# Optimization experiments

Measured on AMD Instinct MI355X. Metric: run time of the kernel, lower is better.

Reference implementation:

```python
import jax, jax.numpy as jnp
import numpy as np

# Block structure (mirrors init_kwargs)
K = 8            # number of blocks
BLK = 1024       # per-block in/out width
TOTAL = K * BLK  # total_dim = 8192
INPUT_IDX = [(i * BLK, (i + 1) * BLK) for i in range(K)]
OUTPUT_IDX = [(((i + 1) % K) * BLK, ((i + 1) % K + 1) * BLK) for i in range(K)]
BATCH = 4096


def setup_inputs() -> dict:
    key = jax.random.key(0)
    k1, k2, k3, k4 = jax.random.split(key, 4)
    x = jax.random.normal(k1, (BATCH, TOTAL), dtype=jnp.float32)
    v = jax.random.normal(k2, (BATCH, TOTAL), dtype=jnp.float32)
    # Per-block Linear params; nn.Linear default init ~ U(-1/sqrt(in), 1/sqrt(in))
    bound = 1.0 / np.sqrt(BLK)
    W = jax.random.uniform(k3, (K, BLK, BLK), dtype=jnp.float32, minval=-bound, maxval=bound)  # [K, out, in]
    b = jax.random.uniform(k4, (K, BLK), dtype=jnp.float32, minval=-bound, maxval=bound)
    return {"x": x, "v": v, "W": W, "b": b}


def reference(x, v, W, b):
    # hidden = act(v)
    hidden = jnp.tanh(v)
    # All input blocks are a uniform partition -> batch the K small GEMMs as one grouped contraction.
    h = hidden.reshape(BATCH, K, BLK)                      # [B, K, in]
    y = jnp.einsum("bki,koi->bko", h, W) + b               # [B, K, out]
    # Scatter-accumulate each block output into its padded position, plus residual x.
    result = x
    for i, (o0, o1) in enumerate(OUTPUT_IDX):
        result = result.at[:, o0:o1].add(y[:, i])
    return result
```

## Files before the change

kernel.cpp:

```cpp
#include <hip/hip_runtime.h>
#include <hip/hip_bf16.h>
#include <stdint.h>

#define BATCH 4096
#define KGRP  8
#define BLK   1024
#define TOTAL 8192

typedef __attribute__((ext_vector_type(8))) short short8;
typedef __attribute__((ext_vector_type(4))) float f32x4;

#define AS1 __attribute__((address_space(1)))
#define AS3 __attribute__((address_space(3)))


__device__ __forceinline__ unsigned short f2bf(float f) {
    union { float f; uint32_t u; } c; c.f = f;
    uint32_t u = c.u;
    u += 0x7fffu + ((u >> 16) & 1u);
    return (unsigned short)(u >> 16);
}

__device__ __forceinline__ float fast_tanh(float x) {
    float e = __expf(2.0f * x);
    return 1.0f - 2.0f / (e + 1.0f);
}


__global__ void k_prep(const float4* __restrict__ v, ushort4* __restrict__ H,
                       const float4* __restrict__ W, ushort4* __restrict__ Wb) {
    const int b = blockIdx.x;
    if (b < 2048) {
        const int n4 = BATCH * TOTAL / 4;
        for (int i = b * 256 + threadIdx.x; i < n4; i += 2048 * 256) {
            float4 f = v[i];
            ushort4 o;
            o.x = f2bf(fast_tanh(f.x)); o.y = f2bf(fast_tanh(f.y));
            o.z = f2bf(fast_tanh(f.z)); o.w = f2bf(fast_tanh(f.w));
            H[i] = o;
        }
    } else {
        const int n4 = KGRP * BLK * BLK / 4;
        for (int i = (b - 2048) * 256 + threadIdx.x; i < n4; i += 512 * 256) {
            float4 f = W[i];
            ushort4 o;
            o.x = f2bf(f.x); o.y = f2bf(f.y); o.z = f2bf(f.z); o.w = f2bf(f.w);
            Wb[i] = o;
        }
    }
}


__device__ __forceinline__ void gload16(const unsigned short* src, char* dst) {
    __builtin_amdgcn_global_load_lds((const AS1 uint32_t*)src, (AS3 uint32_t*)dst, 16, 0, 0);
}

template<int N> __device__ __forceinline__ void waitvm() {
    if constexpr (N == 0)      asm volatile("s_waitcnt vmcnt(0)" ::: "memory");
    else if constexpr (N == 3) asm volatile("s_waitcnt vmcnt(3)" ::: "memory");
}

template<bool ST, int W, int CUR>
__device__ __forceinline__ void tile3(int kt, char* ldsp,
                                      uint32_t aRowB, uint32_t bRowB,
                                      f32x4 (*acc)[4],
                                      const unsigned short* Asrc, const unsigned short* Bsrc,
                                      uint32_t sdst) {
    constexpr uint32_t bufb = (uint32_t)(CUR * 24576);
    constexpr uint32_t stgb = (uint32_t)(((CUR + 2) % 3) * 24576);
    const char* Lb = ldsp + bufb;

    if constexpr (ST) {
        gload16(Asrc + (size_t)(kt + 2) * 32, ldsp + stgb + sdst);
        gload16(Bsrc + (size_t)(kt + 2) * 32, ldsp + stgb + 8192u + sdst);
        gload16(Bsrc + (size_t)128 * BLK + (size_t)(kt + 2) * 32, ldsp + stgb + 16384u + sdst);
    }

    short8 bfr[4], am0[2], am1[2];
#pragma unroll
    for (int n = 0; n < 4; ++n)
        bfr[n] = *(const short8*)(Lb + bRowB + n * 1024);
#pragma unroll
    for (int i = 0; i < 2; ++i)
        am0[i] = *(const short8*)(Lb + aRowB + i * 1024);
#pragma unroll
    for (int i = 0; i < 2; ++i)
        am1[i] = *(const short8*)(Lb + aRowB + (2 + i) * 1024);

    __builtin_amdgcn_s_setprio(1);
#pragma unroll
    for (int i = 0; i < 2; ++i)
#pragma unroll
        for (int n = 0; n < 4; ++n)
            acc[i][n] = __builtin_amdgcn_mfma_f32_16x16x32_bf16(am0[i], bfr[n], acc[i][n], 0, 0, 0);
#pragma unroll
    for (int i = 0; i < 2; ++i)
#pragma unroll
        for (int n = 0; n < 4; ++n)
            acc[2 + i][n] = __builtin_amdgcn_mfma_f32_16x16x32_bf16(am1[i], bfr[n], acc[2 + i][n], 0, 0, 0);
    __builtin_amdgcn_s_setprio(0);

    if constexpr (W >= 0) {
        waitvm<W>();
        __builtin_amdgcn_s_barrier();
        __builtin_amdgcn_sched_barrier(0);
    }
}

__global__ __launch_bounds__(512, 4)
void k_gemm(const unsigned short* __restrict__ H, const unsigned short* __restrict__ Wb,
            const float* __restrict__ x, const float* __restrict__ bias,
            float* __restrict__ out) {
    __shared__ __attribute__((aligned(1024))) char lds[73728];
    char* ldsp = lds;

    const int bid   = blockIdx.x;
    const int g     = bid & 7;
    const int slot  = bid >> 3;
    const int mtile = slot >> 2;
    const int ntile = slot & 3;

    const int tid  = threadIdx.x;
    const int lane = tid & 63;
    const int w    = tid >> 6;
    const int wr   = w >> 2;
    const int wc   = w & 3;

    const uint32_t kc    = ((uint32_t)((lane >> 4) ^ ((lane >> 1) & 3))) << 4;
    const uint32_t aRowB = (uint32_t)(wr * 64 + (lane & 15)) * 64u + kc;
    const uint32_t bRowB = 8192u + (uint32_t)(wc * 64 + (lane & 15)) * 64u + kc;

    const int sCol = ((lane & 3) ^ ((lane >> 3) & 3)) << 3;
    const unsigned short* Asrc = H + (size_t)(mtile * 128 + w * 16 + (lane >> 2)) * TOTAL
                                   + (size_t)g * BLK + sCol;
    const unsigned short* Bsrc = Wb + (size_t)g * BLK * BLK
                                    + (size_t)(ntile * 256 + w * 16 + (lane >> 2)) * BLK + sCol;
    const uint32_t sdst = (uint32_t)(w << 10);

    f32x4 acc[4][4];
#pragma unroll
    for (int m = 0; m < 4; ++m)
#pragma unroll
        for (int n = 0; n < 4; ++n) acc[m][n] = (f32x4){0.f, 0.f, 0.f, 0.f};

    gload16(Asrc + 0, ldsp + 0u + sdst);
    gload16(Bsrc + 0, ldsp + 8192u + sdst);
    gload16(Bsrc + (size_t)128 * BLK, ldsp + 16384u + sdst);
    gload16(Asrc + 32, ldsp + 24576u + sdst);
    gload16(Bsrc + 32, ldsp + 24576u + 8192u + sdst);
    gload16(Bsrc + (size_t)128 * BLK + 32, ldsp + 24576u + 16384u + sdst);
    waitvm<3>();
    __builtin_amdgcn_s_barrier();
    __builtin_amdgcn_sched_barrier(0);

#pragma unroll 1
    for (int kt = 0; kt < 30; kt += 3) {
        tile3<true, 3, 0>(kt,     ldsp, aRowB, bRowB, acc, Asrc, Bsrc, sdst);
        tile3<true, 3, 1>(kt + 1, ldsp, aRowB, bRowB, acc, Asrc, Bsrc, sdst);
        tile3<true, 3, 2>(kt + 2, ldsp, aRowB, bRowB, acc, Asrc, Bsrc, sdst);
    }
    tile3<false, 0, 0>(30, ldsp, aRowB, bRowB, acc, Asrc, Bsrc, sdst);
    tile3<false, -1, 1>(31, ldsp, aRowB, bRowB, acc, Asrc, Bsrc, sdst);

    __builtin_amdgcn_s_barrier();

    const int gout = (g + 1) & 7;
    const int q    = lane >> 4;
    const int cl   = lane & 15;
    const int row0 = mtile * 128 + wr * 64;
    const int col0 = ntile * 256 + wc * 64;
    char* eb = ldsp + (uint32_t)w * 4352u;
    const float4 bias4 = *(const float4*)&bias[g * BLK + col0 + cl * 4];

#pragma unroll
    for (int m = 0; m < 4; ++m) {
#pragma unroll
        for (int n = 0; n < 4; ++n)
#pragma unroll
            for (int j = 0; j < 4; ++j)
                *(float*)(eb + (q * 4 + j) * 272 + (n * 16 + cl) * 4) = acc[m][n][j];
        asm volatile("s_waitcnt lgkmcnt(0)" ::: "memory");
        __builtin_amdgcn_sched_barrier(0);
#pragma unroll
        for (int i = 0; i < 4; ++i) {
            f32x4 vv = *(const f32x4*)(eb + (q + 4 * i) * 272 + cl * 16);
            const int r = row0 + m * 16 + q + 4 * i;
            const size_t idx = (size_t)r * TOTAL + (size_t)gout * BLK + col0 + cl * 4;
            const float4 xv = *(const float4*)&x[idx];
            float4 o;
            o.x = xv.x + bias4.x + vv[0];
            o.y = xv.y + bias4.y + vv[1];
            o.z = xv.z + bias4.z + vv[2];
            o.w = xv.w + bias4.w + vv[3];
            *(float4*)&out[idx] = o;
        }
        asm volatile("s_waitcnt lgkmcnt(0)" ::: "memory");
        __builtin_amdgcn_sched_barrier(0);
    }
}


__global__ void k_naive(const float* __restrict__ x, const float* __restrict__ v,
                        const float* __restrict__ W, const float* __restrict__ b,
                        float* __restrict__ out) {
    __shared__ float hv[BLK];
    const int bid = blockIdx.x;
    const int quarter = bid & 3;
    const int g = (bid >> 2) & 7;
    const int row = bid >> 5;
    for (int i = threadIdx.x; i < BLK; i += 256)
        hv[i] = tanhf(v[(size_t)row * TOTAL + g * BLK + i]);
    __syncthreads();
    const int o = quarter * 256 + threadIdx.x;
    const float* wrow = W + ((size_t)g * BLK + o) * BLK;
    float s = 0.f;
    for (int i = 0; i < BLK; ++i) s += hv[i] * wrow[i];
    const size_t oi = (size_t)row * TOTAL + (size_t)((g + 1) & 7) * BLK + o;
    out[oi] = x[oi] + b[g * BLK + o] + s;
}


extern "C" void kernel_launch(void* const* d_in, const int* in_sizes, int n_in,
                              void* d_out, int out_size, void* d_ws, size_t ws_size,
                              hipStream_t stream) {
    const float* x = (const float*)d_in[0];
    const float* v = (const float*)d_in[1];
    const float* W = (const float*)d_in[2];
    const float* b = (const float*)d_in[3];
    float* out = (float*)d_out;

    const size_t needH = (size_t)BATCH * TOTAL * sizeof(unsigned short);
    const size_t needW = (size_t)KGRP * BLK * BLK * sizeof(unsigned short);

    if (ws_size >= needH + needW) {
        unsigned short* H  = (unsigned short*)d_ws;
        unsigned short* Wb = (unsigned short*)((char*)d_ws + needH);
        k_prep<<<2560, 256, 0, stream>>>((const float4*)v, (ushort4*)H,
                                         (const float4*)W, (ushort4*)Wb);
        k_gemm<<<1024, 512, 0, stream>>>(H, Wb, x, b, out);
    } else {
        k_naive<<<BATCH * KGRP * 4, 256, 0, stream>>>(x, v, W, b, out);
    }
}
```

Before: 157.7 us.

## Fuse tanh activation into GEMM A-operand loading and read weights directly from global

Removes the separate pass that writes tanh(v) as a bf16 intermediate. The main kernel now loads fp32 v, applies tanh, converts to bf16 and stores it into double-buffered LDS as the A operand, with register prefetch two k-steps ahead. B fragments (bf16 weights) are read straight from global memory into registers instead of being staged through LDS. The tile shape changes to 64x512 per block, with each wave owning a 64x64 output slab. This saves writing and re-reading a 64MB intermediate, but adds register-path global loads for B that depend on L2 reuse, and re-reads each v tile once per N-tile.

Result: slower. 216.3 us (+37.1%).

```diff
diff --git a/kernel.cpp b/kernel.cpp
--- a/kernel.cpp
+++ b/kernel.cpp
@@ -9,9 +9,6 @@
 
 typedef __attribute__((ext_vector_type(8))) short short8;
 typedef __attribute__((ext_vector_type(4))) float f32x4;
-
-#define AS1 __attribute__((address_space(1)))
-#define AS3 __attribute__((address_space(3)))
 
 
 __device__ __forceinline__ unsigned short f2bf(float f) {
@@ -26,116 +23,94 @@
     return 1.0f - 2.0f / (e + 1.0f);
 }
 
-
-__global__ void k_prep(const float4* __restrict__ v, ushort4* __restrict__ H,
-                       const float4* __restrict__ W, ushort4* __restrict__ Wb) {
-    const int b = blockIdx.x;
-    if (b < 2048) {
-        const int n4 = BATCH * TOTAL / 4;
-        for (int i = b * 256 + threadIdx.x; i < n4; i += 2048 * 256) {
-            float4 f = v[i];
-            ushort4 o;
-            o.x = f2bf(fast_tanh(f.x)); o.y = f2bf(fast_tanh(f.y));
-            o.z = f2bf(fast_tanh(f.z)); o.w = f2bf(fast_tanh(f.w));
-            H[i] = o;
-        }
-    } else {
-        const int n4 = KGRP * BLK * BLK / 4;
-        for (int i = (b - 2048) * 256 + threadIdx.x; i < n4; i += 512 * 256) {
-            float4 f = W[i];
-            ushort4 o;
-            o.x = f2bf(f.x); o.y = f2bf(f.y); o.z = f2bf(f.z); o.w = f2bf(f.w);
-            Wb[i] = o;
-        }
-    }
-}
-
-
-__device__ __forceinline__ void gload16(const unsigned short* src, char* dst) {
-    __builtin_amdgcn_global_load_lds((const AS1 uint32_t*)src, (AS3 uint32_t*)dst, 16, 0, 0);
-}
-
-template<int N> __device__ __forceinline__ void waitvm() {
-    if constexpr (N == 0)      asm volatile("s_waitcnt vmcnt(0)" ::: "memory");
-    else if constexpr (N == 3) asm volatile("s_waitcnt vmcnt(3)" ::: "memory");
-}
-
-template<bool ST, int W, int CUR>
-__device__ __forceinline__ void tile3(int kt, char* ldsp,
-                                      uint32_t aRowB, uint32_t bRowB,
-                                      f32x4 (*acc)[4],
-                                      const unsigned short* Asrc, const unsigned short* Bsrc,
-                                      uint32_t sdst) {
-    constexpr uint32_t bufb = (uint32_t)(CUR * 24576);
-    constexpr uint32_t stgb = (uint32_t)(((CUR + 2) % 3) * 24576);
-    const char* Lb = ldsp + bufb;
+__device__ __forceinline__ void barrier_tile() {
+    asm volatile("s_waitcnt lgkmcnt(0)" ::: "memory");
+    __builtin_amdgcn_s_barrier();
+    __builtin_amdgcn_sched_barrier(0);
+}
+
+
+__global__ void k_wcast(const float4* __restrict__ W, ushort4* __restrict__ Wb) {
+    const int n4 = KGRP * BLK * BLK / 4;
+    for (int i = blockIdx.x * 256 + threadIdx.x; i < n4; i += 1024 * 256) {
+        float4 f = W[i];
+        ushort4 o;
+        o.x = f2bf(f.x); o.y = f2bf(f.y); o.z = f2bf(f.z); o.w = f2bf(f.w);
+        Wb[i] = o;
+    }
+}
+
+
+template<bool ST, bool ISSV, bool LAST>
+__device__ __forceinline__ void tile_f(int kt, char* ldsp,
+                                       uint32_t aRd, uint32_t aWr,
+                                       const float* vsrc, const unsigned short* bsrc,
+                                       float4& vCons, float4& vLoad,
+                                       f32x4 (*acc)[4]) {
+    const uint32_t cur = (uint32_t)(kt & 1) * 4096u;
+    const uint32_t oth = cur ^ 4096u;
+
+    short8 bf[4];
+#pragma unroll
+    for (int nf = 0; nf < 4; ++nf)
+        bf[nf] = *(const short8*)(bsrc + (size_t)(nf * 16) * BLK + kt * 32);
+
+    if constexpr (ISSV)
+        vLoad = *(const float4*)(vsrc + (kt + 2) * 32);
+
+    short8 am[4];
+#pragma unroll
+    for (int mf = 0; mf < 4; ++mf)
+        am[mf] = *(const short8*)(ldsp + cur + mf * 1024u + aRd);
 
     if constexpr (ST) {
-        gload16(Asrc + (size_t)(kt + 2) * 32, ldsp + stgb + sdst);
-        gload16(Bsrc + (size_t)(kt + 2) * 32, ldsp + stgb + 8192u + sdst);
-        gload16(Bsrc + (size_t)128 * BLK + (size_t)(kt + 2) * 32, ldsp + stgb + 16384u + sdst);
-    }
-
-    short8 bfr[4], am0[2], am1[2];
-#pragma unroll
-    for (int n = 0; n < 4; ++n)
-        bfr[n] = *(const short8*)(Lb + bRowB + n * 1024);
-#pragma unroll
-    for (int i = 0; i < 2; ++i)
-        am0[i] = *(const short8*)(Lb + aRowB + i * 1024);
-#pragma unroll
-    for (int i = 0; i < 2; ++i)
-        am1[i] = *(const short8*)(Lb + aRowB + (2 + i) * 1024);
+        ushort4 o;
+        o.x = f2bf(fast_tanh(vCons.x));
+        o.y = f2bf(fast_tanh(vCons.y));
+        o.z = f2bf(fast_tanh(vCons.z));
+        o.w = f2bf(fast_tanh(vCons.w));
+        *(ushort4*)(ldsp + oth + aWr) = o;
+    }
 
     __builtin_amdgcn_s_setprio(1);
 #pragma unroll
-    for (int i = 0; i < 2; ++i)
-#pragma unroll
-        for (int n = 0; n < 4; ++n)
-            acc[i][n] = __builtin_amdgcn_mfma_f32_16x16x32_bf16(am0[i], bfr[n], acc[i][n], 0, 0, 0);
-#pragma unroll
-    for (int i = 0; i < 2; ++i)
-#pragma unroll
-        for (int n = 0; n < 4; ++n)
-            acc[2 + i][n] = __builtin_amdgcn_mfma_f32_16x16x32_bf16(am1[i], bfr[n], acc[2 + i][n], 0, 0, 0);
+    for (int mf = 0; mf < 4; ++mf)
+#pragma unroll
+        for (int nf = 0; nf < 4; ++nf)
+            acc[mf][nf] = __builtin_amdgcn_mfma_f32_16x16x32_bf16(am[mf], bf[nf], acc[mf][nf], 0, 0, 0);
     __builtin_amdgcn_s_setprio(0);
 
-    if constexpr (W >= 0) {
-        waitvm<W>();
-        __builtin_amdgcn_s_barrier();
-        __builtin_amdgcn_sched_barrier(0);
-    }
+    if constexpr (!LAST) barrier_tile();
 }
 
 __global__ __launch_bounds__(512, 4)
-void k_gemm(const unsigned short* __restrict__ H, const unsigned short* __restrict__ Wb,
+void k_main(const float* __restrict__ v, const unsigned short* __restrict__ Wb,
             const float* __restrict__ x, const float* __restrict__ bias,
             float* __restrict__ out) {
-    __shared__ __attribute__((aligned(1024))) char lds[73728];
+    __shared__ __attribute__((aligned(1024))) char lds[43008];
     char* ldsp = lds;
 
     const int bid   = blockIdx.x;
     const int g     = bid & 7;
     const int slot  = bid >> 3;
-    const int mtile = slot >> 2;
-    const int ntile = slot & 3;
+    const int mtile = slot >> 1;
+    const int ntile = slot & 1;
+    const int gout  = (g + 1) & 7;
 
     const int tid  = threadIdx.x;
     const int lane = tid & 63;
     const int w    = tid >> 6;
-    const int wr   = w >> 2;
-    const int wc   = w & 3;
-
-    const uint32_t kc    = ((uint32_t)((lane >> 4) ^ ((lane >> 1) & 3))) << 4;
-    const uint32_t aRowB = (uint32_t)(wr * 64 + (lane & 15)) * 64u + kc;
-    const uint32_t bRowB = 8192u + (uint32_t)(wc * 64 + (lane & 15)) * 64u + kc;
-
-    const int sCol = ((lane & 3) ^ ((lane >> 3) & 3)) << 3;
-    const unsigned short* Asrc = H + (size_t)(mtile * 128 + w * 16 + (lane >> 2)) * TOTAL
-                                   + (size_t)g * BLK + sCol;
-    const unsigned short* Bsrc = Wb + (size_t)g * BLK * BLK
-                                    + (size_t)(ntile * 256 + w * 16 + (lane >> 2)) * BLK + sCol;
-    const uint32_t sdst = (uint32_t)(w << 10);
+
+    const uint32_t aRd = (uint32_t)(lane & 15) * 64u +
+                         (((uint32_t)((lane >> 4) ^ ((lane >> 1) & 3))) << 4);
+    const int wrow = tid >> 3;
+    const int h    = tid & 7;
+    const uint32_t aWr = (uint32_t)wrow * 64u +
+                         (((uint32_t)(((h >> 1) ^ ((wrow >> 1) & 3)))) << 4) +
+                         (uint32_t)(h & 1) * 8u;
+    const float* vsrc = v + (size_t)(mtile * 64 + wrow) * TOTAL + (size_t)g * BLK + h * 4;
+    const unsigned short* bsrc = Wb + ((size_t)g * BLK + ntile * 512 + w * 64 + (lane & 15)) * BLK
+                                    + (lane >> 4) * 8;
 
     f32x4 acc[4][4];
 #pragma unroll
@@ -143,33 +118,32 @@
 #pragma unroll
         for (int n = 0; n < 4; ++n) acc[m][n] = (f32x4){0.f, 0.f, 0.f, 0.f};
 
-    gload16(Asrc + 0, ldsp + 0u + sdst);
-    gload16(Bsrc + 0, ldsp + 8192u + sdst);
-    gload16(Bsrc + (size_t)128 * BLK, ldsp + 16384u + sdst);
-    gload16(Asrc + 32, ldsp + 24576u + sdst);
-    gload16(Bsrc + 32, ldsp + 24576u + 8192u + sdst);
-    gload16(Bsrc + (size_t)128 * BLK + 32, ldsp + 24576u + 16384u + sdst);
-    waitvm<3>();
-    __builtin_amdgcn_s_barrier();
-    __builtin_amdgcn_sched_barrier(0);
+    {
+        float4 f0 = *(const float4*)(vsrc);
+        ushort4 o;
+        o.x = f2bf(fast_tanh(f0.x));
+        o.y = f2bf(fast_tanh(f0.y));
+        o.z = f2bf(fast_tanh(f0.z));
+        o.w = f2bf(fast_tanh(f0.w));
+        *(ushort4*)(ldsp + aWr) = o;
+    }
+    float4 vA = *(const float4*)(vsrc + 32);
+    float4 vB;
+    barrier_tile();
 
 #pragma unroll 1
-    for (int kt = 0; kt < 30; kt += 3) {
-        tile3<true, 3, 0>(kt,     ldsp, aRowB, bRowB, acc, Asrc, Bsrc, sdst);
-        tile3<true, 3, 1>(kt + 1, ldsp, aRowB, bRowB, acc, Asrc, Bsrc, sdst);
-        tile3<true, 3, 2>(kt + 2, ldsp, aRowB, bRowB, acc, Asrc, Bsrc, sdst);
-    }
-    tile3<false, 0, 0>(30, ldsp, aRowB, bRowB, acc, Asrc, Bsrc, sdst);
-    tile3<false, -1, 1>(31, ldsp, aRowB, bRowB, acc, Asrc, Bsrc, sdst);
-
-    __builtin_amdgcn_s_barrier();
-
-    const int gout = (g + 1) & 7;
-    const int q    = lane >> 4;
-    const int cl   = lane & 15;
-    const int row0 = mtile * 128 + wr * 64;
-    const int col0 = ntile * 256 + wc * 64;
-    char* eb = ldsp + (uint32_t)w * 4352u;
+    for (int k2 = 0; k2 < 15; ++k2) {
+        const int kt = k2 * 2;
+        tile_f<true, true, false>(kt,     ldsp, aRd, aWr, vsrc, bsrc, vA, vB, acc);
+        tile_f<true, true, false>(kt + 1, ldsp, aRd, aWr, vsrc, bsrc, vB, vA, acc);
+    }
+    tile_f<true,  false, false>(30, ldsp, aRd, aWr, vsrc, bsrc, vA, vB, acc);
+    tile_f<false, false, true >(31, ldsp, aRd, aWr, vsrc, bsrc, vB, vA, acc);
+
+    const int q  = lane >> 4;
+    const int cl = lane & 15;
+    const int col0 = ntile * 512 + w * 64;
+    char* eb = ldsp + 8192u + (uint32_t)w * 4352u;
     const float4 bias4 = *(const float4*)&bias[g * BLK + col0 + cl * 4];
 
 #pragma unroll
@@ -184,7 +158,7 @@
 #pragma unroll
         for (int i = 0; i < 4; ++i) {
             f32x4 vv = *(const f32x4*)(eb + (q + 4 * i) * 272 + cl * 16);
-            const int r = row0 + m * 16 + q + 4 * i;
+            const int r = mtile * 64 + m * 16 + q + 4 * i;
             const size_t idx = (size_t)r * TOTAL + (size_t)gout * BLK + col0 + cl * 4;
             const float4 xv = *(const float4*)&x[idx];
             float4 o;
@@ -229,15 +203,12 @@
     const float* b = (const float*)d_in[3];
     float* out = (float*)d_out;
 
-    const size_t needH = (size_t)BATCH * TOTAL * sizeof(unsigned short);
     const size_t needW = (size_t)KGRP * BLK * BLK * sizeof(unsigned short);
 
-    if (ws_size >= needH + needW) {
-        unsigned short* H  = (unsigned short*)d_ws;
-        unsigned short* Wb = (unsigned short*)((char*)d_ws + needH);
-        k_prep<<<2560, 256, 0, stream>>>((const float4*)v, (ushort4*)H,
-                                         (const float4*)W, (ushort4*)Wb);
-        k_gemm<<<1024, 512, 0, stream>>>(H, Wb, x, b, out);
+    if (ws_size >= needW) {
+        unsigned short* Wb = (unsigned short*)d_ws;
+        k_wcast<<<1024, 256, 0, stream>>>((const float4*)W, (ushort4*)Wb);
+        k_main<<<1024, 512, 0, stream>>>(v, Wb, x, b, out);
     } else {
         k_naive<<<BATCH * KGRP * 4, 256, 0, stream>>>(x, v, W, b, out);
     }
```
